# Kernel tuning notes

Measured on AMD Instinct MI355X. Metric: run time of the kernel, lower is better.

## Reference

```python
import jax, jax.numpy as jnp
import numpy as np

V = 32000   # num_tokens
D = 1024    # dim
L = 4       # depth
H = 8       # heads
B = 2       # batch
T = 2048    # seq_len (divisible by H)
SCALE = (D // H) ** -0.5  # scale uses dim//heads as in source
EPS = 1e-5
NEG_SLOPE = 0.01  # LeakyReLU default


def layernorm(x, g, b):
    mu = jnp.mean(x, axis=-1, keepdims=True)
    var = jnp.mean(jnp.square(x - mu), axis=-1, keepdims=True)
    return (x - mu) * jax.lax.rsqrt(var + EPS) * g + b


def setup_inputs() -> dict:
    key = jax.random.key(0)
    ks = jax.random.split(key, 8)
    s = 0.02
    f = lambda k, shape: jax.random.normal(k, shape, jnp.float32) * s
    return {
        "x": jax.random.randint(ks[0], (B, T), 0, V),
        "token_emb": f(ks[1], (V, D)),
        "ln1_g": jnp.ones((L, D), jnp.float32), "ln1_b": jnp.zeros((L, D), jnp.float32),
        "wqkv": f(ks[2], (L, D, 3 * D)),
        "wout_w": f(ks[3], (L, D, D)), "wout_b": jnp.zeros((L, D), jnp.float32),
        "ln2_g": jnp.ones((L, D), jnp.float32), "ln2_b": jnp.zeros((L, D), jnp.float32),
        "ff1_w": f(ks[4], (L, D, 4 * D)), "ff1_b": jnp.zeros((L, 4 * D), jnp.float32),
        "ff2_w": f(ks[5], (L, 4 * D, D)), "ff2_b": jnp.zeros((L, D), jnp.float32),
        "logit_w": f(ks[6], (D, V)), "logit_b": jnp.zeros((V,), jnp.float32),
    }


def reference(x, token_emb, ln1_g, ln1_b, wqkv, wout_w, wout_b,
              ln2_g, ln2_b, ff1_w, ff1_b, ff2_w, ff2_b, logit_w, logit_b):
    h = token_emb[x]  # [B, T, D]
    for i in range(L):
        # --- Residual(PreNorm(SelfAttention)) ---
        y = layernorm(h, ln1_g[i], ln1_b[i])
        qkv = y @ wqkv[i]                      # [B, T, 3D]
        q, k, v = jnp.split(qkv, 3, axis=-1)
        # faithful to source: reshape(b, -1, h, e) with e = full dim -> heads
        # partition the sequence into H strided groups, head-dim = D
        rs = lambda t: t.reshape(B, T // H, H, D).transpose(0, 2, 1, 3)  # [B, H, T/H, D]
        q, k, v = rs(q), rs(k), rs(v)
        dots = jnp.einsum('bhid,bhjd->bhij', q, k) * SCALE
        attn = jax.nn.softmax(dots, axis=-1)
        o = jnp.einsum('bhij,bhjd->bhid', attn, v)
        o = o.transpose(0, 2, 1, 3).reshape(B, T, D)
        h = h + (o @ wout_w[i] + wout_b[i])
        # --- Residual(PreNorm(FeedForward)) ---
        y = layernorm(h, ln2_g[i], ln2_b[i])
        y = y @ ff1_w[i] + ff1_b[i]
        y = jnp.where(y >= 0, y, NEG_SLOPE * y)  # LeakyReLU
        h = h + (y @ ff2_w[i] + ff2_b[i])
    return h @ logit_w + logit_b  # [B, T, V]
```

## Files before the change

kernel.cpp:

```cpp
#include <hip/hip_runtime.h>

#define DD 1024
#define LL 4
#define HH 8
#define BB 2
#define TT 2048
#define VV 32000
#define SCALE_QK 0.08838834764831845f

typedef __bf16 bf16x8 __attribute__((ext_vector_type(8)));
typedef __bf16 bf16x4 __attribute__((ext_vector_type(4)));
typedef float  f32x4  __attribute__((ext_vector_type(4)));

__device__ __forceinline__ void gload_lds16(const void* g, void* l) {
  __builtin_amdgcn_global_load_lds((const __attribute__((address_space(1))) void*)g,
                                   (__attribute__((address_space(3))) void*)l, 16, 0, 0);
}

template<int MODE>
__global__ __launch_bounds__(256, 2)
void gemm_mt(const __bf16* __restrict__ A, long ldA, long aSB, long aSH,
             const __bf16* __restrict__ Bt, long ldB, long bSB, long bSH,
             void* __restrict__ Cv, long ldC, long cSB, long cSH,
             const float* __restrict__ bias,
             const float* __restrict__ res, long ldR,
             int K)
{
  extern __shared__ __attribute__((aligned(16))) char smem[];

  int zbh = blockIdx.z;
  if (MODE == 5) {
    const int kc = zbh >> 4;
    zbh &= 15;
    A  += (size_t)kc * K;
    Bt += (size_t)kc * K;
  }
  const int zb = zbh >> 3, zh = zbh & 7;
  A  += (size_t)zb * aSB + (size_t)zh * aSH;
  Bt += (size_t)zb * bSB + (size_t)zh * bSH;
  const size_t cOff = (size_t)zb * cSB + (size_t)zh * cSH;

  const int nbx = gridDim.x, nby = gridDim.y;
  const int nwg = nbx * nby;
  const int fid = blockIdx.y * nbx + blockIdx.x;
  const int q8 = nwg >> 3, r8 = nwg & 7;
  const int xcd = fid & 7, idx = fid >> 3;
  const int swz = (xcd < r8 ? xcd * (q8 + 1) : r8 * (q8 + 1) + (xcd - r8) * q8) + idx;
  const int bx = swz / nby, by = swz - bx * nby;
  const int m0 = by * 256, n0 = bx * 128;

  const int tid = threadIdx.x;
  const int wv = tid >> 6, ln = tid & 63;
  const int wm = wv >> 1, wn = wv & 1;

  const int usA = (ln & 7) ^ (ln >> 3);
  const int rsA = wv * 64 + 2 * (ln >> 3) + (usA >> 2);
  const int ksA = (usA & 3) * 8;
  const __bf16* pA0 = A + (size_t)(m0 + rsA) * ldA + ksA;
  const int usB = (tid & 7) ^ ((tid >> 3) & 7);
  const int rsB = 2 * (tid >> 3) + (usB >> 2);
  const int ksB = (usB & 3) * 8;
  const __bf16* pB0 = Bt + (size_t)(n0 + rsB) * ldB + ksB;

  const int lr = ln & 15;
  const int gfr = ((((ln & 1) << 2) | ((ln >> 4) & 3)) ^ ((ln >> 1) & 7)) << 4;
  const int aR = (wm * 64 + (lr >> 1)) * 128 + gfr;
  const int bR = 49152 + (wn * 32 + (lr >> 1)) * 128 + gfr;

  f32x4 acc[8][4] = {};
  const int NT = K >> 5;

#define STG(sl) { \
    char* da = smem + (sl) * 16384 + wv * 4096 + ln * 16; \
    gload_lds16(pA0,            da); \
    gload_lds16(pA0 + 16 * ldA, da + 1024); \
    gload_lds16(pA0 + 32 * ldA, da + 2048); \
    gload_lds16(pA0 + 48 * ldA, da + 3072); \
    char* db = smem + 49152 + (sl) * 8192 + tid * 16; \
    gload_lds16(pB0,            db); \
    gload_lds16(pB0 + 64 * ldB, db + 4096); \
    pA0 += 32; pB0 += 32; }

  STG(0);
  if (NT > 1) {
    STG(1);
    asm volatile("s_waitcnt vmcnt(6)" ::: "memory");
  } else {
    asm volatile("s_waitcnt vmcnt(0)" ::: "memory");
  }
  __builtin_amdgcn_s_barrier();

  int sc = 0, sn = 1, sf = 2;
  for (int t = 0; t < NT; ++t) {
    if (t + 2 < NT) STG(sf);
    const char* aBase = smem + sc * 16384 + aR;
    const char* bBase = smem + sc * 8192 + bR;
    bf16x8 a[8], b[4];
#pragma unroll
    for (int j = 0; j < 4; j++) b[j] = *(const bf16x8*)(bBase + j * 1024);
#pragma unroll
    for (int i = 0; i < 8; i++) a[i] = *(const bf16x8*)(aBase + i * 1024);
    __builtin_amdgcn_s_setprio(1);
#pragma unroll
    for (int i = 0; i < 8; i++)
#pragma unroll
      for (int j = 0; j < 4; j++)
        acc[i][j] = __builtin_amdgcn_mfma_f32_16x16x32_bf16(a[i], b[j], acc[i][j], 0, 0, 0);
    __builtin_amdgcn_s_setprio(0);
    if (t + 1 < NT) {
      if (t + 2 < NT) { asm volatile("s_waitcnt vmcnt(6)" ::: "memory"); }
      else            { asm volatile("s_waitcnt vmcnt(0)" ::: "memory"); }
      __builtin_amdgcn_sched_barrier(0);
      __builtin_amdgcn_s_barrier();
    }
    const int tmp = sc; sc = sn; sn = sf; sf = tmp;
  }
#undef STG

  const int rb = m0 + wm * 128 + (ln >> 4) * 4;
  const int cb = n0 + wn * 64 + lr;
#pragma unroll
  for (int i = 0; i < 8; i++)
#pragma unroll
    for (int j = 0; j < 4; j++) {
      const int col = cb + j * 16;
#pragma unroll
      for (int r = 0; r < 4; r++) {
        const int row = rb + i * 16 + r;
        float v = acc[i][j][r];
        const size_t ci = cOff + (size_t)row * ldC + col;
        if (MODE == 0)      ((__bf16*)Cv)[ci] = (__bf16)v;
        else if (MODE == 1) ((float*)Cv)[ci] = v;
        else if (MODE == 2) ((float*)Cv)[ci] = v + bias[col] + res[(size_t)row * ldR + col];
        else if (MODE == 3) { v += bias[col]; ((__bf16*)Cv)[ci] = (__bf16)(v >= 0.f ? v : 0.01f * v); }
        else if (MODE == 4) ((float*)Cv)[ci] = v + bias[col];
        else if (MODE == 5) atomicAdd(&((float*)Cv)[ci], v);
      }
    }
}

__global__ void wtrans(const float* __restrict__ W, __bf16* __restrict__ Wt, int K, int N)
{
  const size_t zo = (size_t)blockIdx.z * K * N;
  __shared__ float t[32][33];
  const int n0 = blockIdx.x * 32, k0 = blockIdx.y * 32;
  const int tx = threadIdx.x, ty = threadIdx.y;
#pragma unroll
  for (int r = 0; r < 4; r++)
    t[ty + r * 8][tx] = W[zo + (size_t)(k0 + ty + r * 8) * N + n0 + tx];
  __syncthreads();
#pragma unroll
  for (int r = 0; r < 4; r++)
    Wt[zo + (size_t)(n0 + ty + r * 8) * K + k0 + tx] = (__bf16)t[tx][ty + r * 8];
}

__global__ void vtrans(const __bf16* __restrict__ qkv, __bf16* __restrict__ Vt)
{
  const int z = blockIdx.z, bb = z >> 3, hh = z & 7;
  const __bf16* src = qkv + ((size_t)bb * TT + hh) * (3 * DD) + 2 * DD;
  __bf16* dst = Vt + (size_t)z * DD * 256;
  __shared__ __bf16 t[32][33];
  const int n0 = blockIdx.x * 32, i0 = blockIdx.y * 32;
  const int tx = threadIdx.x, ty = threadIdx.y;
#pragma unroll
  for (int r = 0; r < 4; r++)
    t[ty + r * 8][tx] = src[(size_t)(i0 + ty + r * 8) * (HH * 3 * DD) + n0 + tx];
  __syncthreads();
#pragma unroll
  for (int r = 0; r < 4; r++)
    dst[(size_t)(n0 + ty + r * 8) * 256 + i0 + tx] = t[tx][ty + r * 8];
}

__global__ void embed_k(const int* __restrict__ x, const float* __restrict__ emb, float* __restrict__ h)
{
  const int row = blockIdx.x;
  const int tok = x[row];
  ((float4*)(h + (size_t)row * DD))[threadIdx.x] = ((const float4*)(emb + (size_t)tok * DD))[threadIdx.x];
}

__global__ void ln_rows(const float* __restrict__ x, const float* __restrict__ g,
                        const float* __restrict__ b, __bf16* __restrict__ y)
{
  const int row = blockIdx.x, t = threadIdx.x;
  const int wv = t >> 6, ln = t & 63;
  const float4 v = ((const float4*)(x + (size_t)row * DD))[t];
  float s  = v.x + v.y + v.z + v.w;
  float ss = v.x * v.x + v.y * v.y + v.z * v.z + v.w * v.w;
#pragma unroll
  for (int o = 32; o; o >>= 1) { s += __shfl_xor(s, o); ss += __shfl_xor(ss, o); }
  __shared__ float rs_[4], rss_[4];
  if (!ln) { rs_[wv] = s; rss_[wv] = ss; }
  __syncthreads();
  s  = rs_[0] + rs_[1] + rs_[2] + rs_[3];
  ss = rss_[0] + rss_[1] + rss_[2] + rss_[3];
  const float mu  = s * (1.0f / DD);
  const float var = ss * (1.0f / DD) - mu * mu;
  const float r   = rsqrtf(var + 1e-5f);
  const float4 gv = ((const float4*)g)[t];
  const float4 bv = ((const float4*)b)[t];
  bf16x4 o = { (__bf16)((v.x - mu) * r * gv.x + bv.x),
               (__bf16)((v.y - mu) * r * gv.y + bv.y),
               (__bf16)((v.z - mu) * r * gv.z + bv.z),
               (__bf16)((v.w - mu) * r * gv.w + bv.w) };
  ((bf16x4*)(y + (size_t)row * DD))[t] = o;
}

__global__ void softmax256(const float* __restrict__ S, __bf16* __restrict__ P)
{
  const int row = blockIdx.x, t = threadIdx.x;
  const int wv = t >> 6, ln = t & 63;
  const float v = S[(size_t)row * 256 + t] * SCALE_QK;
  float m = v;
#pragma unroll
  for (int o = 32; o; o >>= 1) m = fmaxf(m, __shfl_xor(m, o));
  __shared__ float red[8];
  if (!ln) red[wv] = m;
  __syncthreads();
  m = fmaxf(fmaxf(red[0], red[1]), fmaxf(red[2], red[3]));
  const float e = __expf(v - m);
  float s = e;
#pragma unroll
  for (int o = 32; o; o >>= 1) s += __shfl_xor(s, o);
  if (!ln) red[4 + wv] = s;
  __syncthreads();
  s = red[4] + red[5] + red[6] + red[7];
  P[(size_t)row * 256 + t] = (__bf16)(e / s);
}

__global__ void f2bf(const float* __restrict__ h, __bf16* __restrict__ y)
{
  const size_t i = (size_t)blockIdx.x * 256 + threadIdx.x;
  const float4 a = ((const float4*)h)[2 * i];
  const float4 b = ((const float4*)h)[2 * i + 1];
  bf16x8 o = { (__bf16)a.x, (__bf16)a.y, (__bf16)a.z, (__bf16)a.w,
               (__bf16)b.x, (__bf16)b.y, (__bf16)b.z, (__bf16)b.w };
  ((bf16x8*)y)[i] = o;
}

template<int MODE>
static void G(const __bf16* A, long ldA, long aSB, long aSH,
              const __bf16* Bt, long ldB, long bSB, long bSH,
              void* C, long ldC, long cSB, long cSH,
              const float* bias, const float* res, long ldR,
              int M, int N, int K, int Z, hipStream_t s)
{
  hipFuncSetAttribute((const void*)gemm_mt<MODE>,
                      hipFuncAttributeMaxDynamicSharedMemorySize, 73728);
  gemm_mt<MODE><<<dim3(N / 128, M / 256, Z), 256, 73728, s>>>(
      A, ldA, aSB, aSH, Bt, ldB, bSB, bSH, C, ldC, cSB, cSH, bias, res, ldR, K);
}

extern "C" void kernel_launch(void* const* d_in, const int* in_sizes, int n_in,
                              void* d_out, int out_size, void* d_ws, size_t ws_size,
                              hipStream_t stream)
{
  const int*   x       = (const int*)  d_in[0];
  const float* emb     = (const float*)d_in[1];
  const float* ln1_g   = (const float*)d_in[2];
  const float* ln1_b   = (const float*)d_in[3];
  const float* wqkv    = (const float*)d_in[4];
  const float* wout_w  = (const float*)d_in[5];
  const float* wout_b  = (const float*)d_in[6];
  const float* ln2_g   = (const float*)d_in[7];
  const float* ln2_b   = (const float*)d_in[8];
  const float* ff1_w   = (const float*)d_in[9];
  const float* ff1_b   = (const float*)d_in[10];
  const float* ff2_w   = (const float*)d_in[11];
  const float* ff2_b   = (const float*)d_in[12];
  const float* logit_w = (const float*)d_in[13];
  const float* logit_b = (const float*)d_in[14];
  float* out = (float*)d_out;

  char* w = (char*)d_ws;
  size_t off = 0;
  auto take = [&](size_t bytes) { void* p = w + off; off += (bytes + 255) & ~(size_t)255; return p; };
  __bf16* wqkvT = (__bf16*)take((size_t)LL * 3 * DD * DD * 2);
  __bf16* woutT = (__bf16*)take((size_t)LL * DD * DD * 2);
  __bf16* ff1T  = (__bf16*)take((size_t)LL * 4 * DD * DD * 2);
  __bf16* ff2T  = (__bf16*)take((size_t)LL * DD * 4 * DD * 2);
  __bf16* logT  = (__bf16*)take((size_t)VV * DD * 2);
  float*  h     = (float*) take((size_t)BB * TT * DD * 4);
  __bf16* ybf   = (__bf16*)take((size_t)BB * TT * DD * 2);
  __bf16* qkvbf = (__bf16*)take((size_t)BB * TT * 3 * DD * 2);
  float*  Smat  = (float*) take((size_t)BB * HH * 256 * 256 * 4);
  __bf16* Pbf   = (__bf16*)take((size_t)BB * HH * 256 * 256 * 2);
  __bf16* Vt    = (__bf16*)take((size_t)BB * HH * DD * 256 * 2);
  __bf16* Obf   = (__bf16*)take((size_t)BB * TT * DD * 2);
  __bf16* midbf = (__bf16*)take((size_t)BB * TT * 4 * DD * 2);
  if (ws_size < off) return;

  const dim3 tb(32, 8);
  wtrans<<<dim3(3 * DD / 32, DD / 32, LL), tb, 0, stream>>>(wqkv,   wqkvT, DD, 3 * DD);
  wtrans<<<dim3(DD / 32,     DD / 32, LL), tb, 0, stream>>>(wout_w, woutT, DD, DD);
  wtrans<<<dim3(4 * DD / 32, DD / 32, LL), tb, 0, stream>>>(ff1_w,  ff1T,  DD, 4 * DD);
  wtrans<<<dim3(DD / 32, 4 * DD / 32, LL), tb, 0, stream>>>(ff2_w,  ff2T,  4 * DD, DD);
  wtrans<<<dim3(VV / 32,     DD / 32, 1),  tb, 0, stream>>>(logit_w, logT, DD, VV);

  const int M = BB * TT;
  embed_k<<<M, 256, 0, stream>>>(x, emb, h);

  for (int l = 0; l < LL; l++) {
    ln_rows<<<M, 256, 0, stream>>>(h, ln1_g + l * DD, ln1_b + l * DD, ybf);
    G<0>(ybf, DD, 0, 0, wqkvT + (size_t)l * 3 * DD * DD, DD, 0, 0,
         qkvbf, 3 * DD, 0, 0, nullptr, nullptr, 0, M, 3 * DD, DD, 1, stream);
    hipMemsetAsync(Smat, 0, (size_t)BB * HH * 256 * 256 * 4, stream);
    G<5>(qkvbf, HH * 3 * DD, (long)TT * 3 * DD, 3 * DD,
         qkvbf + DD, HH * 3 * DD, (long)TT * 3 * DD, 3 * DD,
         Smat, 256, (long)HH * 256 * 256, 256 * 256,
         nullptr, nullptr, 0, 256, 256, DD / 4, 4 * BB * HH, stream);
    softmax256<<<BB * HH * 256, 256, 0, stream>>>(Smat, Pbf);
    vtrans<<<dim3(DD / 32, 256 / 32, BB * HH), tb, 0, stream>>>(qkvbf, Vt);
    G<0>(Pbf, 256, (long)HH * 256 * 256, 256 * 256,
         Vt, 256, (long)HH * DD * 256, (long)DD * 256,
         Obf, HH * DD, (long)TT * DD, DD,
         nullptr, nullptr, 0, 256, DD, 256, BB * HH, stream);
    G<2>(Obf, DD, 0, 0, woutT + (size_t)l * DD * DD, DD, 0, 0,
         h, DD, 0, 0, wout_b + l * DD, h, DD, M, DD, DD, 1, stream);
    ln_rows<<<M, 256, 0, stream>>>(h, ln2_g + l * DD, ln2_b + l * DD, ybf);
    G<3>(ybf, DD, 0, 0, ff1T + (size_t)l * 4 * DD * DD, DD, 0, 0,
         midbf, 4 * DD, 0, 0, ff1_b + (size_t)l * 4 * DD, nullptr, 0, M, 4 * DD, DD, 1, stream);
    G<2>(midbf, 4 * DD, 0, 0, ff2T + (size_t)l * DD * 4 * DD, 4 * DD, 0, 0,
         h, DD, 0, 0, ff2_b + l * DD, h, DD, M, DD, 4 * DD, 1, stream);
  }

  f2bf<<<(M * DD / 8) / 256, 256, 0, stream>>>(h, ybf);
  G<4>(ybf, DD, 0, 0, logT, DD, 0, 0,
       out, VV, 0, 0, logit_b, nullptr, 0, M, VV, DD, 1, stream);
}
```

Measured before the change: 1.460 ms.

## Switch GEMM inner loop to 32x32x16 MFMA with new LDS swizzle

Replaces the 16x16x32 bf16 MFMA tiling (8x4 fragments per wave) with 32x32x16 MFMA (4x2 fragments, two K-halves per 32-wide K step). The shared-memory staging layout, XOR swizzle, fragment load addresses and epilogue row/column mapping are rewritten to match. The aim is fewer LDS fragment reads per FLOP and a higher-throughput MFMA shape. The risk is new LDS bank conflicts or a wrong swizzle/epilogue mapping.

```diff
diff --git a/kernel.cpp b/kernel.cpp
--- a/kernel.cpp
+++ b/kernel.cpp
@@ -11,6 +11,7 @@
 typedef __bf16 bf16x8 __attribute__((ext_vector_type(8)));
 typedef __bf16 bf16x4 __attribute__((ext_vector_type(4)));
 typedef float  f32x4  __attribute__((ext_vector_type(4)));
+typedef float  f32x16 __attribute__((ext_vector_type(16)));
 
 __device__ __forceinline__ void gload_lds16(const void* g, void* l) {
   __builtin_amdgcn_global_load_lds((const __attribute__((address_space(1))) void*)g,
@@ -19,12 +20,12 @@
 
 template<int MODE>
 __global__ __launch_bounds__(256, 2)
-void gemm_mt(const __bf16* __restrict__ A, long ldA, long aSB, long aSH,
-             const __bf16* __restrict__ Bt, long ldB, long bSB, long bSH,
-             void* __restrict__ Cv, long ldC, long cSB, long cSH,
-             const float* __restrict__ bias,
-             const float* __restrict__ res, long ldR,
-             int K)
+void gemm_w(const __bf16* __restrict__ A, long ldA, long aSB, long aSH,
+            const __bf16* __restrict__ Bt, long ldB, long bSB, long bSH,
+            void* __restrict__ Cv, long ldC, long cSB, long cSH,
+            const float* __restrict__ bias,
+            const float* __restrict__ res, long ldR,
+            int K)
 {
   extern __shared__ __attribute__((aligned(16))) char smem[];
 
@@ -53,33 +54,30 @@
   const int wv = tid >> 6, ln = tid & 63;
   const int wm = wv >> 1, wn = wv & 1;
 
-  const int usA = (ln & 7) ^ (ln >> 3);
-  const int rsA = wv * 64 + 2 * (ln >> 3) + (usA >> 2);
-  const int ksA = (usA & 3) * 8;
-  const __bf16* pA0 = A + (size_t)(m0 + rsA) * ldA + ksA;
-  const int usB = (tid & 7) ^ ((tid >> 3) & 7);
-  const int rsB = 2 * (tid >> 3) + (usB >> 2);
-  const int ksB = (usB & 3) * 8;
-  const __bf16* pB0 = Bt + (size_t)(n0 + rsB) * ldB + ksB;
-
-  const int lr = ln & 15;
-  const int gfr = ((((ln & 1) << 2) | ((ln >> 4) & 3)) ^ ((ln >> 1) & 7)) << 4;
-  const int aR = (wm * 64 + (lr >> 1)) * 128 + gfr;
-  const int bR = 49152 + (wn * 32 + (lr >> 1)) * 128 + gfr;
-
-  f32x4 acc[8][4] = {};
+  const int gq = (ln & 3) ^ ((ln >> 2) & 3);
+  const int rq = tid >> 2;
+  const __bf16* pA = A  + (size_t)(m0 + rq) * ldA + gq * 8;
+  const __bf16* pB = Bt + (size_t)(n0 + rq) * ldB + gq * 8;
+
+  const int l31 = ln & 31, lhi = ln >> 5, l3 = ln & 3;
+  const int colK0 = ((lhi) ^ l3) * 16;
+  const int colK1 = ((2 + lhi) ^ l3) * 16;
+  const int aBase = (wm * 128 + l31) * 64;
+  const int bBase = (wn * 64 + l31) * 64;
+
+  f32x16 acc[4][2] = {};
   const int NT = K >> 5;
 
 #define STG(sl) { \
-    char* da = smem + (sl) * 16384 + wv * 4096 + ln * 16; \
-    gload_lds16(pA0,            da); \
-    gload_lds16(pA0 + 16 * ldA, da + 1024); \
-    gload_lds16(pA0 + 32 * ldA, da + 2048); \
-    gload_lds16(pA0 + 48 * ldA, da + 3072); \
+    char* da = smem + (sl) * 16384 + tid * 16; \
+    gload_lds16(pA,             da); \
+    gload_lds16(pA +  64 * ldA, da + 4096); \
+    gload_lds16(pA + 128 * ldA, da + 8192); \
+    gload_lds16(pA + 192 * ldA, da + 12288); \
     char* db = smem + 49152 + (sl) * 8192 + tid * 16; \
-    gload_lds16(pB0,            db); \
-    gload_lds16(pB0 + 64 * ldB, db + 4096); \
-    pA0 += 32; pB0 += 32; }
+    gload_lds16(pB,             db); \
+    gload_lds16(pB +  64 * ldB, db + 4096); \
+    pA += 32; pB += 32; }
 
   STG(0);
   if (NT > 1) {
@@ -93,19 +91,28 @@
   int sc = 0, sn = 1, sf = 2;
   for (int t = 0; t < NT; ++t) {
     if (t + 2 < NT) STG(sf);
-    const char* aBase = smem + sc * 16384 + aR;
-    const char* bBase = smem + sc * 8192 + bR;
-    bf16x8 a[8], b[4];
-#pragma unroll
-    for (int j = 0; j < 4; j++) b[j] = *(const bf16x8*)(bBase + j * 1024);
-#pragma unroll
-    for (int i = 0; i < 8; i++) a[i] = *(const bf16x8*)(aBase + i * 1024);
+    const char* ua = smem + sc * 16384 + aBase;
+    const char* ub = smem + 49152 + sc * 8192 + bBase;
+    bf16x8 a0[4], b0[2], a1[4], b1[2];
+#pragma unroll
+    for (int i = 0; i < 4; i++) a0[i] = *(const bf16x8*)(ua + i * 2048 + colK0);
+#pragma unroll
+    for (int j = 0; j < 2; j++) b0[j] = *(const bf16x8*)(ub + j * 2048 + colK0);
+#pragma unroll
+    for (int i = 0; i < 4; i++) a1[i] = *(const bf16x8*)(ua + i * 2048 + colK1);
+#pragma unroll
+    for (int j = 0; j < 2; j++) b1[j] = *(const bf16x8*)(ub + j * 2048 + colK1);
     __builtin_amdgcn_s_setprio(1);
 #pragma unroll
-    for (int i = 0; i < 8; i++)
-#pragma unroll
-      for (int j = 0; j < 4; j++)
-        acc[i][j] = __builtin_amdgcn_mfma_f32_16x16x32_bf16(a[i], b[j], acc[i][j], 0, 0, 0);
+    for (int i = 0; i < 4; i++)
+#pragma unroll
+      for (int j = 0; j < 2; j++)
+        acc[i][j] = __builtin_amdgcn_mfma_f32_32x32x16_bf16(a0[i], b0[j], acc[i][j], 0, 0, 0);
+#pragma unroll
+    for (int i = 0; i < 4; i++)
+#pragma unroll
+      for (int j = 0; j < 2; j++)
+        acc[i][j] = __builtin_amdgcn_mfma_f32_32x32x16_bf16(a1[i], b1[j], acc[i][j], 0, 0, 0);
     __builtin_amdgcn_s_setprio(0);
     if (t + 1 < NT) {
       if (t + 2 < NT) { asm volatile("s_waitcnt vmcnt(6)" ::: "memory"); }
@@ -117,16 +124,16 @@
   }
 #undef STG
 
-  const int rb = m0 + wm * 128 + (ln >> 4) * 4;
-  const int cb = n0 + wn * 64 + lr;
-#pragma unroll
-  for (int i = 0; i < 8; i++)
-#pragma unroll
-    for (int j = 0; j < 4; j++) {
-      const int col = cb + j * 16;
-#pragma unroll
-      for (int r = 0; r < 4; r++) {
-        const int row = rb + i * 16 + r;
+  const int cb = n0 + wn * 64 + l31;
+  const int rbase = m0 + wm * 128 + 4 * lhi;
+#pragma unroll
+  for (int i = 0; i < 4; i++)
+#pragma unroll
+    for (int j = 0; j < 2; j++) {
+      const int col = cb + j * 32;
+#pragma unroll
+      for (int r = 0; r < 16; r++) {
+        const int row = rbase + i * 32 + (r & 3) + 8 * (r >> 2);
         float v = acc[i][j][r];
         const size_t ci = cOff + (size_t)row * ldC + col;
         if (MODE == 0)      ((__bf16*)Cv)[ci] = (__bf16)v;
@@ -244,9 +251,9 @@
               const float* bias, const float* res, long ldR,
               int M, int N, int K, int Z, hipStream_t s)
 {
-  hipFuncSetAttribute((const void*)gemm_mt<MODE>,
+  hipFuncSetAttribute((const void*)gemm_w<MODE>,
                       hipFuncAttributeMaxDynamicSharedMemorySize, 73728);
-  gemm_mt<MODE><<<dim3(N / 128, M / 256, Z), 256, 73728, s>>>(
+  gemm_w<MODE><<<dim3(N / 128, M / 256, Z), 256, 73728, s>>>(
       A, ldA, aSB, aSH, Bt, ldB, bSB, bSH, C, ldC, cSB, cSH, bias, res, ldR, K);
 }
 
```

After: 1.648 ms. 1.13x slower.
